# Kernel tuning notes

Measured on AMD Instinct MI355X. Metric: run time of the kernel, lower is better.

The kernel has to match this reference:

```python
import jax, jax.numpy as jnp
import numpy as np

B, DV, DT, H, G, E = 4096, 1024, 1024, 1024, 4096, 8
D = DV + DT  # fused dim = 2048


def setup_inputs() -> dict:
    key = jax.random.key(0)
    ks = jax.random.split(key, 8)
    s = 0.02
    return {
        "vision_cls": jax.random.normal(ks[0], (B, DV), jnp.float32),
        "text_cls": jax.random.normal(ks[1], (B, DT), jnp.float32),
        "W1_imm": jax.random.normal(ks[2], (E, D, H), jnp.float32) * s,
        "b1_imm": jnp.zeros((E, H), jnp.float32),
        "W2_imm": jax.random.normal(ks[3], (E, H, 1), jnp.float32) * s,
        "b2_imm": jnp.zeros((E, 1), jnp.float32),
        "W1_gene": jax.random.normal(ks[4], (E, D, H), jnp.float32) * s,
        "b1_gene": jnp.zeros((E, H), jnp.float32),
        "W2_gene": jax.random.normal(ks[5], (E, H, G), jnp.float32) * s,
        "b2_gene": jnp.zeros((E, G), jnp.float32),
        "organ_idx": jax.random.randint(ks[6], (B,), 0, E, jnp.int32),
    }


def reference(vision_cls, text_cls, W1_imm, b1_imm, W2_imm, b2_imm,
              W1_gene, b1_gene, W2_gene, b2_gene, organ_idx):
    # fused features [B, D]
    fused = jnp.concatenate([vision_cls, text_cls], axis=-1)
    # Dense MoE reference: run every organ head on the full batch, then
    # select each sample's routed output (same math as the per-group
    # gather -> MLP -> scatter in the original; dropout is eval-mode identity).
    h_i = jax.nn.relu(jnp.einsum('bd,edh->ebh', fused, W1_imm) + b1_imm[:, None, :])
    imm_all = jnp.einsum('ebh,eh->eb', h_i, W2_imm[:, :, 0]) + b2_imm[:, :1]  # [E,B]
    h_g = jax.nn.relu(jnp.einsum('bd,edh->ebh', fused, W1_gene) + b1_gene[:, None, :])
    gene_all = jnp.einsum('ebh,ehg->ebg', h_g, W2_gene) + b2_gene[:, None, :]  # [E,B,G]
    bidx = jnp.arange(fused.shape[0])
    immune = imm_all[organ_idx, bidx]      # [B]
    gene = gene_all[organ_idx, bidx]       # [B,G] (uniform gene_dim -> no padding needed)
    return immune, gene, vision_cls, text_cls
```

## Files before the change

### kernel.cpp

```cpp
#include <hip/hip_runtime.h>


#define B_N 4096
#define DV  1024
#define DT  1024
#define DD  2048
#define HH  1024
#define GG  4096
#define EE  8
#define BM  128
#define MAXRB 40
#define PERM_N (MAXRB * BM)
#define LDT 40

typedef __bf16 bf16x8 __attribute__((ext_vector_type(8)));
typedef float f32x4 __attribute__((ext_vector_type(4)));
typedef unsigned short u16x4v __attribute__((ext_vector_type(4)));
typedef unsigned short u16x8v __attribute__((ext_vector_type(8)));

#define H_CNT 0
#define H_FIL 8
#define H_OFF 16
#define H_NRB 24
#define H_BLK 32

static __device__ __forceinline__ unsigned short f2bf(float f) {
  unsigned u = __builtin_bit_cast(unsigned, f);
  u += 0x7fffu + ((u >> 16) & 1u);
  return (unsigned short)(u >> 16);
}
static __device__ __forceinline__ float bf2f(unsigned short s) {
  return __builtin_bit_cast(float, (unsigned)s << 16);
}

static __device__ __forceinline__ void gload16(const void* g, void* l) {
  __builtin_amdgcn_global_load_lds(
      (const __attribute__((address_space(1))) unsigned int*)g,
      (__attribute__((address_space(3))) unsigned int*)l, 16, 0, 0);
}

__global__ void s_init(int* hdr, int* perm) {
  int i = blockIdx.x * 256 + threadIdx.x;
  if (i < 128) hdr[i] = 0;
  if (i < PERM_N) perm[i] = -1;
}
__global__ void s_count(const int* organ, int* hdr) {
  int b = blockIdx.x * 256 + threadIdx.x;
  if (b < B_N) atomicAdd(&hdr[H_CNT + organ[b]], 1);
}
__global__ void s_scan(int* hdr) {
  if (blockIdx.x == 0 && threadIdx.x == 0) {
    int acc = 0;
    for (int e = 0; e < EE; ++e) {
      hdr[H_OFF + e] = acc;
      int nb = (hdr[H_CNT + e] + BM - 1) >> 7;
      int rb0 = acc >> 7;
      for (int i = 0; i < nb; ++i) hdr[H_BLK + rb0 + i] = e;
      acc += nb << 7;
    }
    hdr[H_NRB] = acc >> 7;
  }
}
__global__ void s_scatter(const int* organ, int* hdr, int* perm) {
  int b = blockIdx.x * 256 + threadIdx.x;
  if (b < B_N) {
    int e = organ[b];
    int slot = hdr[H_OFF + e] + atomicAdd(&hdr[H_FIL + e], 1);
    perm[slot] = b;
  }
}

__global__ __launch_bounds__(256) void w_cvt(const float* __restrict__ in,
                                             unsigned short* __restrict__ out,
                                             int K, int N) {
  __shared__ unsigned short ls[64][72];
  const int tid = threadIdx.x;
  const int K0 = blockIdx.y << 6, N0 = blockIdx.x << 6;
  const size_t ein = (size_t)blockIdx.z * K * N;
  const int kr = tid >> 4, n0 = (tid & 15) << 2;
#pragma unroll
  for (int p = 0; p < 4; ++p) {
    int k = (p << 4) + kr;
    float4 f = *(const float4*)&in[ein + (size_t)(K0 + k) * N + N0 + n0];
    ls[n0 + 0][k] = f2bf(f.x);
    ls[n0 + 1][k] = f2bf(f.y);
    ls[n0 + 2][k] = f2bf(f.z);
    ls[n0 + 3][k] = f2bf(f.w);
  }
  __syncthreads();
  const int n = tid >> 2, kc = (tid & 3) << 4;
  u16x8v a = *(const u16x8v*)&ls[n][kc];
  u16x8v b = *(const u16x8v*)&ls[n][kc + 8];
  size_t o = (size_t)blockIdx.z * N * K + (size_t)(N0 + n) * K + K0 + kc;
  *(u16x8v*)&out[o] = a;
  *(u16x8v*)&out[o + 8] = b;
}

__global__ void a_build(const float* __restrict__ vis, const float* __restrict__ txt,
                        const int* __restrict__ hdr, const int* __restrict__ perm,
                        unsigned short* __restrict__ Abuf) {
  const int r = blockIdx.x;
  if (r >= hdr[H_NRB] * BM) return;
  const int smp = perm[r];
  const int c = threadIdx.x << 3;
  u16x8v v;
  if (smp >= 0) {
    const float* src = (c < DV) ? vis + (size_t)smp * DV + c
                                : txt + (size_t)smp * DT + (c - DV);
    float4 a = *(const float4*)src, b = *(const float4*)(src + 4);
    v[0] = f2bf(a.x); v[1] = f2bf(a.y); v[2] = f2bf(a.z); v[3] = f2bf(a.w);
    v[4] = f2bf(b.x); v[5] = f2bf(b.y); v[6] = f2bf(b.z); v[7] = f2bf(b.w);
  } else {
#pragma unroll
    for (int i = 0; i < 8; ++i) v[i] = 0;
  }
  *(u16x8v*)&Abuf[(size_t)r * DD + c] = v;
}

__global__ __launch_bounds__(256) void gemm_l1_v1(
    const unsigned short* __restrict__ Abuf,
    const unsigned short* __restrict__ W1i_t, const unsigned short* __restrict__ W1g_t,
    const float* __restrict__ b1i, const float* __restrict__ b1g,
    const int* __restrict__ hdr,
    unsigned short* __restrict__ H1, unsigned short* __restrict__ H2) {
  const int rb = blockIdx.x;
  if (rb >= hdr[H_NRB]) return;
  const int head = blockIdx.y >> 3;
  const int cb = (blockIdx.y & 7) << 7;
  const int e = hdr[H_BLK + rb];
  const unsigned short* Wt = (head ? W1g_t : W1i_t) + (size_t)e * HH * DD;
  const float* bias = (head ? b1g : b1i) + e * HH;
  unsigned short* Hout = head ? H2 : H1;

  __shared__ __align__(16) unsigned short smem[16384];
  const int tid = threadIdx.x;
  const int lane = tid & 63, wave = tid >> 6;
  const int wr = (wave >> 1) << 6, wc = (wave & 1) << 6;
  const int lr = lane & 15, lk = (lane >> 4) << 3;
  const unsigned short* Arow0 = Abuf + (size_t)rb * BM * DD;

  f32x4 acc[4][4];
#pragma unroll
  for (int m = 0; m < 4; ++m)
#pragma unroll
    for (int n = 0; n < 4; ++n) acc[m][n] = (f32x4){0.f, 0.f, 0.f, 0.f};

  for (int k0 = 0; k0 < DD; k0 += 32) {
#pragma unroll
    for (int j = 0; j < 2; ++j) {
      int s = j * 256 + tid;
      int row = s >> 2, kq = (s & 3) << 3;
      gload16(Arow0 + (size_t)row * DD + k0 + kq,
              smem + ((j * 256 + (tid & 192)) << 3));
    }
#pragma unroll
    for (int j = 0; j < 2; ++j) {
      int s = j * 256 + tid;
      int row = s >> 2, kq = (s & 3) << 3;
      gload16(Wt + (size_t)(cb + row) * DD + k0 + kq,
              smem + 4096 + ((j * 256 + (tid & 192)) << 3));
    }
    __syncthreads();
    bf16x8 af[4], bfr[4];
#pragma unroll
    for (int m = 0; m < 4; ++m)
      af[m] = *(const bf16x8*)&smem[(wr + m * 16 + lr) * 32 + lk];
#pragma unroll
    for (int n = 0; n < 4; ++n)
      bfr[n] = *(const bf16x8*)&smem[4096 + (wc + n * 16 + lr) * 32 + lk];
#pragma unroll
    for (int m = 0; m < 4; ++m)
#pragma unroll
      for (int n = 0; n < 4; ++n)
        acc[m][n] = __builtin_amdgcn_mfma_f32_16x16x32_bf16(af[m], bfr[n], acc[m][n], 0, 0, 0);
    __syncthreads();
  }

  const int r0l = wr + ((lane >> 4) << 2);
#pragma unroll
  for (int n = 0; n < 4; ++n) {
    const int col = wc + n * 16 + lr;
    const float bv = bias[cb + col];
#pragma unroll
    for (int m = 0; m < 4; ++m)
#pragma unroll
      for (int v = 0; v < 4; ++v) {
        int row = r0l + m * 16 + v;
        float x = acc[m][n][v] + bv;
        x = x > 0.f ? x : 0.f;
        smem[((row << 7) + col) ^ ((row & 7) << 3)] = f2bf(x);
      }
  }
  __syncthreads();
#pragma unroll
  for (int c = 0; c < 8; ++c) {
    int q = c * 256 + tid;
    int row = q >> 4, ch = q & 15;
    int off = ((row << 7) + (ch << 3)) ^ ((row & 7) << 3);
    u16x8v val = *(const u16x8v*)&smem[off];
    *(u16x8v*)&Hout[(size_t)(rb * BM + row) * HH + cb + (ch << 3)] = val;
  }
}

__global__ __launch_bounds__(256) void gemm_l2_v1(
    const unsigned short* __restrict__ H2, const unsigned short* __restrict__ W2gt,
    const float* __restrict__ b2g, const int* __restrict__ hdr,
    const int* __restrict__ perm, float* __restrict__ outg) {
  const int rb = blockIdx.x;
  if (rb >= hdr[H_NRB]) return;
  const int cb = blockIdx.y << 7;
  const int e = hdr[H_BLK + rb];
  const unsigned short* Wt = W2gt + (size_t)e * GG * HH;

  __shared__ __align__(16) unsigned short smem[16384];
  const int tid = threadIdx.x;
  const int lane = tid & 63, wave = tid >> 6;
  const int wr = (wave >> 1) << 6, wc = (wave & 1) << 6;
  const int lr = lane & 15, lk = (lane >> 4) << 3;
  const unsigned short* Arow0 = H2 + (size_t)rb * BM * HH;

  f32x4 acc[4][4];
#pragma unroll
  for (int m = 0; m < 4; ++m)
#pragma unroll
    for (int n = 0; n < 4; ++n) acc[m][n] = (f32x4){0.f, 0.f, 0.f, 0.f};

  for (int k0 = 0; k0 < HH; k0 += 32) {
#pragma unroll
    for (int j = 0; j < 2; ++j) {
      int s = j * 256 + tid;
      int row = s >> 2, kq = (s & 3) << 3;
      gload16(Arow0 + (size_t)row * HH + k0 + kq,
              smem + ((j * 256 + (tid & 192)) << 3));
    }
#pragma unroll
    for (int j = 0; j < 2; ++j) {
      int s = j * 256 + tid;
      int row = s >> 2, kq = (s & 3) << 3;
      gload16(Wt + (size_t)(cb + row) * HH + k0 + kq,
              smem + 4096 + ((j * 256 + (tid & 192)) << 3));
    }
    __syncthreads();
    bf16x8 af[4], bfr[4];
#pragma unroll
    for (int m = 0; m < 4; ++m)
      af[m] = *(const bf16x8*)&smem[(wr + m * 16 + lr) * 32 + lk];
#pragma unroll
    for (int n = 0; n < 4; ++n)
      bfr[n] = *(const bf16x8*)&smem[4096 + (wc + n * 16 + lr) * 32 + lk];
#pragma unroll
    for (int m = 0; m < 4; ++m)
#pragma unroll
      for (int n = 0; n < 4; ++n)
        acc[m][n] = __builtin_amdgcn_mfma_f32_16x16x32_bf16(af[m], bfr[n], acc[m][n], 0, 0, 0);
    __syncthreads();
  }

  const int r0l = wr + ((lane >> 4) << 2);
#pragma unroll
  for (int n = 0; n < 4; ++n) {
    const int col = wc + n * 16 + lr;
    const float bv = b2g[e * GG + cb + col];
#pragma unroll
    for (int m = 0; m < 4; ++m)
#pragma unroll
      for (int v = 0; v < 4; ++v) {
        int row = r0l + m * 16 + v;
        smem[((row << 7) + col) ^ ((row & 7) << 3)] = f2bf(acc[m][n][v] + bv);
      }
  }
  __syncthreads();
#pragma unroll
  for (int c = 0; c < 8; ++c) {
    int q = c * 256 + tid;
    int row = q >> 4, ch = q & 15;
    int sm = perm[rb * BM + row];
    if (sm < 0) continue;
    int off = ((row << 7) + (ch << 3)) ^ ((row & 7) << 3);
    u16x8v val = *(const u16x8v*)&smem[off];
    float4 f0, f1;
    f0.x = bf2f(val[0]); f0.y = bf2f(val[1]); f0.z = bf2f(val[2]); f0.w = bf2f(val[3]);
    f1.x = bf2f(val[4]); f1.y = bf2f(val[5]); f1.z = bf2f(val[6]); f1.w = bf2f(val[7]);
    float* dst = outg + (size_t)sm * GG + cb + (ch << 3);
    *(float4*)dst = f0;
    *(float4*)(dst + 4) = f1;
  }
}

__global__ __launch_bounds__(256) void immune_k(
    const int* __restrict__ hdr, const int* __restrict__ perm,
    const unsigned short* __restrict__ H1, const float* __restrict__ W2,
    const float* __restrict__ b2, float* __restrict__ out) {
  const int nrb = hdr[H_NRB];
  const int r = blockIdx.x * 4 + (threadIdx.x >> 6);
  if (r >= nrb * BM) return;
  const int b = perm[r];
  if (b < 0) return;
  const int e = hdr[H_BLK + (r >> 7)];
  const int lane = threadIdx.x & 63;
  const unsigned short* h = H1 + (size_t)r * HH + lane * 16;
  const float* w = W2 + (size_t)e * HH + lane * 16;
  float s = 0.f;
#pragma unroll
  for (int i = 0; i < 16; ++i) s += bf2f(h[i]) * w[i];
#pragma unroll
  for (int off = 32; off >= 1; off >>= 1) s += __shfl_xor(s, off, 64);
  if (lane == 0) out[b] = s + b2[e];
}

__global__ void copy_vt(const float4* __restrict__ v, const float4* __restrict__ t,
                        float4* __restrict__ ov, float4* __restrict__ ot) {
  const int n4 = B_N * DV / 4;
  for (int i = blockIdx.x * blockDim.x + threadIdx.x; i < n4;
       i += gridDim.x * blockDim.x) {
    ov[i] = v[i];
    ot[i] = t[i];
  }
}

__global__ __launch_bounds__(256) void gemm_l1_v0(
    const float* __restrict__ vis, const float* __restrict__ txt,
    const float* __restrict__ W1, const float* __restrict__ b1,
    const int* __restrict__ hdr, const int* __restrict__ perm,
    unsigned short* __restrict__ Hout) {
  const int nrb = hdr[H_NRB];
  const int rb = blockIdx.x;
  if (rb >= nrb) return;
  const int cb = blockIdx.y << 7;
  const int e = hdr[H_BLK + rb];
  const int tid = threadIdx.x;
  __shared__ unsigned short As[BM * LDT];
  __shared__ unsigned short Bs[BM * LDT];
  const int ar = tid & 127, akg = (tid >> 7) << 4;
  const int smp = perm[rb * BM + ar];
  const int bc = (tid & 31) << 2, bk = (tid >> 5) << 2;
  const float* Wb = W1 + (size_t)e * DD * HH;
  const int wave = tid >> 6, lane = tid & 63;
  const int wr = (wave >> 1) << 6, wc = (wave & 1) << 6;
  const int lr = lane & 15, lk = (lane >> 4) << 3;
  f32x4 acc[4][4];
#pragma unroll
  for (int m = 0; m < 4; ++m)
#pragma unroll
    for (int n = 0; n < 4; ++n) acc[m][n] = (f32x4){0.f, 0.f, 0.f, 0.f};
  for (int k0 = 0; k0 < DD; k0 += 32) {
    {
      const int kk = k0 + akg;
      u16x8v v0, v1;
      if (smp >= 0) {
        const float* src = (kk < DV) ? (vis + (size_t)smp * DV + kk)
                                     : (txt + (size_t)smp * DT + (kk - DV));
#pragma unroll
        for (int i = 0; i < 2; ++i) {
          float4 f = reinterpret_cast<const float4*>(src)[i];
          v0[4 * i + 0] = f2bf(f.x); v0[4 * i + 1] = f2bf(f.y);
          v0[4 * i + 2] = f2bf(f.z); v0[4 * i + 3] = f2bf(f.w);
        }
#pragma unroll
        for (int i = 0; i < 2; ++i) {
          float4 f = reinterpret_cast<const float4*>(src)[2 + i];
          v1[4 * i + 0] = f2bf(f.x); v1[4 * i + 1] = f2bf(f.y);
          v1[4 * i + 2] = f2bf(f.z); v1[4 * i + 3] = f2bf(f.w);
        }
      } else {
#pragma unroll
        for (int i = 0; i < 8; ++i) { v0[i] = 0; v1[i] = 0; }
      }
      *reinterpret_cast<u16x8v*>(&As[ar * LDT + akg]) = v0;
      *reinterpret_cast<u16x8v*>(&As[ar * LDT + akg + 8]) = v1;
    }
    {
      unsigned short bv[4][4];
#pragma unroll
      for (int i = 0; i < 4; ++i) {
        float4 f = *reinterpret_cast<const float4*>(Wb + (size_t)(k0 + bk + i) * HH + cb + bc);
        bv[0][i] = f2bf(f.x); bv[1][i] = f2bf(f.y);
        bv[2][i] = f2bf(f.z); bv[3][i] = f2bf(f.w);
      }
#pragma unroll
      for (int j = 0; j < 4; ++j) {
        u16x4v w; w[0] = bv[j][0]; w[1] = bv[j][1]; w[2] = bv[j][2]; w[3] = bv[j][3];
        *reinterpret_cast<u16x4v*>(&Bs[(bc + j) * LDT + bk]) = w;
      }
    }
    __syncthreads();
    bf16x8 af[4], bfr[4];
#pragma unroll
    for (int m = 0; m < 4; ++m)
      af[m] = *reinterpret_cast<const bf16x8*>(&As[(wr + m * 16 + lr) * LDT + lk]);
#pragma unroll
    for (int n = 0; n < 4; ++n)
      bfr[n] = *reinterpret_cast<const bf16x8*>(&Bs[(wc + n * 16 + lr) * LDT + lk]);
#pragma unroll
    for (int m = 0; m < 4; ++m)
#pragma unroll
      for (int n = 0; n < 4; ++n)
        acc[m][n] = __builtin_amdgcn_mfma_f32_16x16x32_bf16(af[m], bfr[n], acc[m][n], 0, 0, 0);
    __syncthreads();
  }
  const int r0 = rb * BM + wr + ((lane >> 4) << 2);
#pragma unroll
  for (int n = 0; n < 4; ++n) {
    const int col = cb + wc + n * 16 + lr;
    const float bias = b1[e * HH + col];
#pragma unroll
    for (int m = 0; m < 4; ++m)
#pragma unroll
      for (int v = 0; v < 4; ++v) {
        float x = acc[m][n][v] + bias;
        x = x > 0.f ? x : 0.f;
        Hout[(size_t)(r0 + m * 16 + v) * HH + col] = f2bf(x);
      }
  }
}

__global__ __launch_bounds__(256) void gemm_l2_v0(
    const unsigned short* __restrict__ H2, const float* __restrict__ W2,
    const float* __restrict__ b2, const int* __restrict__ hdr,
    const int* __restrict__ perm, float* __restrict__ outg) {
  const int nrb = hdr[H_NRB];
  const int rb = blockIdx.x;
  if (rb >= nrb) return;
  const int cb = blockIdx.y << 7;
  const int e = hdr[H_BLK + rb];
  const int tid = threadIdx.x;
  __shared__ unsigned short As[BM * LDT];
  __shared__ unsigned short Bs[BM * LDT];
  const int ar = tid & 127, akg = (tid >> 7) << 4;
  const unsigned short* Arow = H2 + (size_t)(rb * BM + ar) * HH;
  const int bc = (tid & 31) << 2, bk = (tid >> 5) << 2;
  const float* Wb = W2 + (size_t)e * HH * GG;
  const int wave = tid >> 6, lane = tid & 63;
  const int wr = (wave >> 1) << 6, wc = (wave & 1) << 6;
  const int lr = lane & 15, lk = (lane >> 4) << 3;
  f32x4 acc[4][4];
#pragma unroll
  for (int m = 0; m < 4; ++m)
#pragma unroll
    for (int n = 0; n < 4; ++n) acc[m][n] = (f32x4){0.f, 0.f, 0.f, 0.f};
  for (int k0 = 0; k0 < HH; k0 += 32) {
    {
      u16x8v v0 = *reinterpret_cast<const u16x8v*>(Arow + k0 + akg);
      u16x8v v1 = *reinterpret_cast<const u16x8v*>(Arow + k0 + akg + 8);
      *reinterpret_cast<u16x8v*>(&As[ar * LDT + akg]) = v0;
      *reinterpret_cast<u16x8v*>(&As[ar * LDT + akg + 8]) = v1;
    }
    {
      unsigned short bv[4][4];
#pragma unroll
      for (int i = 0; i < 4; ++i) {
        float4 f = *reinterpret_cast<const float4*>(Wb + (size_t)(k0 + bk + i) * GG + cb + bc);
        bv[0][i] = f2bf(f.x); bv[1][i] = f2bf(f.y);
        bv[2][i] = f2bf(f.z); bv[3][i] = f2bf(f.w);
      }
#pragma unroll
      for (int j = 0; j < 4; ++j) {
        u16x4v w; w[0] = bv[j][0]; w[1] = bv[j][1]; w[2] = bv[j][2]; w[3] = bv[j][3];
        *reinterpret_cast<u16x4v*>(&Bs[(bc + j) * LDT + bk]) = w;
      }
    }
    __syncthreads();
    bf16x8 af[4], bfr[4];
#pragma unroll
    for (int m = 0; m < 4; ++m)
      af[m] = *reinterpret_cast<const bf16x8*>(&As[(wr + m * 16 + lr) * LDT + lk]);
#pragma unroll
    for (int n = 0; n < 4; ++n)
      bfr[n] = *reinterpret_cast<const bf16x8*>(&Bs[(wc + n * 16 + lr) * LDT + lk]);
#pragma unroll
    for (int m = 0; m < 4; ++m)
#pragma unroll
      for (int n = 0; n < 4; ++n)
        acc[m][n] = __builtin_amdgcn_mfma_f32_16x16x32_bf16(af[m], bfr[n], acc[m][n], 0, 0, 0);
    __syncthreads();
  }
  const int r0 = rb * BM + wr + ((lane >> 4) << 2);
#pragma unroll
  for (int m = 0; m < 4; ++m) {
    int sm[4];
#pragma unroll
    for (int v = 0; v < 4; ++v) sm[v] = perm[r0 + m * 16 + v];
#pragma unroll
    for (int n = 0; n < 4; ++n) {
      const int col = cb + wc + n * 16 + lr;
      const float bias = b2[e * GG + col];
#pragma unroll
      for (int v = 0; v < 4; ++v)
        if (sm[v] >= 0) outg[(size_t)sm[v] * GG + col] = acc[m][n][v] + bias;
    }
  }
}

extern "C" void kernel_launch(void* const* d_in, const int* in_sizes, int n_in,
                              void* d_out, int out_size, void* d_ws, size_t ws_size,
                              hipStream_t stream) {
  (void)in_sizes; (void)n_in; (void)out_size;
  const float* vis = (const float*)d_in[0];
  const float* txt = (const float*)d_in[1];
  const float* W1i = (const float*)d_in[2];
  const float* b1i = (const float*)d_in[3];
  const float* W2i = (const float*)d_in[4];
  const float* b2i = (const float*)d_in[5];
  const float* W1g = (const float*)d_in[6];
  const float* b1g = (const float*)d_in[7];
  const float* W2g = (const float*)d_in[8];
  const float* b2g = (const float*)d_in[9];
  const int* organ = (const int*)d_in[10];

  float* out_imm = (float*)d_out;
  float* out_gene = out_imm + B_N;
  float* out_vis = out_gene + (size_t)B_N * GG;
  float* out_txt = out_vis + (size_t)B_N * DV;

  int* hdr = (int*)d_ws;
  int* perm = hdr + 128;

  const size_t OFF_ABUF = 32768;
  const size_t OFF_H1 = OFF_ABUF + (size_t)PERM_N * DD * 2;
  const size_t OFF_H2 = OFF_H1 + (size_t)PERM_N * HH * 2;
  const size_t OFF_W1I = OFF_H2 + (size_t)PERM_N * HH * 2;
  const size_t OFF_W1G = OFF_W1I + (size_t)EE * HH * DD * 2;
  const size_t OFF_W2G = OFF_W1G + (size_t)EE * HH * DD * 2;
  const size_t NEED = OFF_W2G + (size_t)EE * GG * HH * 2;

  s_init<<<PERM_N / 256, 256, 0, stream>>>(hdr, perm);
  s_count<<<B_N / 256, 256, 0, stream>>>(organ, hdr);
  s_scan<<<1, 64, 0, stream>>>(hdr);
  s_scatter<<<B_N / 256, 256, 0, stream>>>(organ, hdr, perm);

  if (ws_size >= NEED) {
    unsigned short* Abuf = (unsigned short*)((char*)d_ws + OFF_ABUF);
    unsigned short* H1 = (unsigned short*)((char*)d_ws + OFF_H1);
    unsigned short* H2 = (unsigned short*)((char*)d_ws + OFF_H2);
    unsigned short* W1i_t = (unsigned short*)((char*)d_ws + OFF_W1I);
    unsigned short* W1g_t = (unsigned short*)((char*)d_ws + OFF_W1G);
    unsigned short* W2g_t = (unsigned short*)((char*)d_ws + OFF_W2G);

    w_cvt<<<dim3(HH / 64, DD / 64, EE), 256, 0, stream>>>(W1i, W1i_t, DD, HH);
    w_cvt<<<dim3(HH / 64, DD / 64, EE), 256, 0, stream>>>(W1g, W1g_t, DD, HH);
    w_cvt<<<dim3(GG / 64, HH / 64, EE), 256, 0, stream>>>(W2g, W2g_t, HH, GG);
    a_build<<<PERM_N, 256, 0, stream>>>(vis, txt, hdr, perm, Abuf);

    gemm_l1_v1<<<dim3(MAXRB, 16), 256, 0, stream>>>(Abuf, W1i_t, W1g_t, b1i, b1g,
                                                    hdr, H1, H2);
    immune_k<<<PERM_N / 4, 256, 0, stream>>>(hdr, perm, H1, W2i, b2i, out_imm);
    gemm_l2_v1<<<dim3(MAXRB, GG / 128), 256, 0, stream>>>(H2, W2g_t, b2g, hdr,
                                                          perm, out_gene);
  } else {
    unsigned short* H1 = (unsigned short*)((char*)d_ws + 32768);
    unsigned short* H2 = H1 + (size_t)PERM_N * HH;
    gemm_l1_v0<<<dim3(MAXRB, HH / 128), 256, 0, stream>>>(vis, txt, W1i, b1i, hdr, perm, H1);
    gemm_l1_v0<<<dim3(MAXRB, HH / 128), 256, 0, stream>>>(vis, txt, W1g, b1g, hdr, perm, H2);
    immune_k<<<PERM_N / 4, 256, 0, stream>>>(hdr, perm, H1, W2i, b2i, out_imm);
    gemm_l2_v0<<<dim3(MAXRB, GG / 128), 256, 0, stream>>>(H2, W2g, b2g, hdr, perm, out_gene);
  }
  copy_vt<<<2048, 256, 0, stream>>>((const float4*)vis, (const float4*)txt,
                                    (float4*)out_vis, (float4*)out_txt);
}
```

Baseline: 311.6 us.

## Merge launches into fused multi-role kernels and double-buffer GEMM main loop

```diff
diff --git a/kernel.cpp b/kernel.cpp
--- a/kernel.cpp
+++ b/kernel.cpp
@@ -32,112 +32,171 @@
 static __device__ __forceinline__ float bf2f(unsigned short s) {
   return __builtin_bit_cast(float, (unsigned)s << 16);
 }
-
 static __device__ __forceinline__ void gload16(const void* g, void* l) {
   __builtin_amdgcn_global_load_lds(
       (const __attribute__((address_space(1))) unsigned int*)g,
       (__attribute__((address_space(3))) unsigned int*)l, 16, 0, 0);
 }
 
-__global__ void s_init(int* hdr, int* perm) {
-  int i = blockIdx.x * 256 + threadIdx.x;
-  if (i < 128) hdr[i] = 0;
-  if (i < PERM_N) perm[i] = -1;
-}
-__global__ void s_count(const int* organ, int* hdr) {
-  int b = blockIdx.x * 256 + threadIdx.x;
-  if (b < B_N) atomicAdd(&hdr[H_CNT + organ[b]], 1);
-}
-__global__ void s_scan(int* hdr) {
-  if (blockIdx.x == 0 && threadIdx.x == 0) {
+__global__ __launch_bounds__(1024) void routing(const int* __restrict__ organ,
+                                                int* __restrict__ hdr,
+                                                int* __restrict__ perm) {
+  __shared__ int cnt[EE], fil[EE], off[EE];
+  const int tid = threadIdx.x;
+  if (tid < EE) { cnt[tid] = 0; fil[tid] = 0; }
+  __syncthreads();
+#pragma unroll
+  for (int i = 0; i < 4; ++i) atomicAdd(&cnt[organ[tid + (i << 10)]], 1);
+#pragma unroll
+  for (int i = 0; i < 5; ++i) perm[tid + (i << 10)] = -1;
+  __syncthreads();
+  if (tid == 0) {
     int acc = 0;
     for (int e = 0; e < EE; ++e) {
+      off[e] = acc;
       hdr[H_OFF + e] = acc;
-      int nb = (hdr[H_CNT + e] + BM - 1) >> 7;
+      hdr[H_CNT + e] = cnt[e];
+      int nb = (cnt[e] + BM - 1) >> 7;
       int rb0 = acc >> 7;
       for (int i = 0; i < nb; ++i) hdr[H_BLK + rb0 + i] = e;
       acc += nb << 7;
     }
     hdr[H_NRB] = acc >> 7;
   }
-}
-__global__ void s_scatter(const int* organ, int* hdr, int* perm) {
-  int b = blockIdx.x * 256 + threadIdx.x;
-  if (b < B_N) {
+  __syncthreads();
+#pragma unroll
+  for (int i = 0; i < 4; ++i) {
+    int b = tid + (i << 10);
     int e = organ[b];
-    int slot = hdr[H_OFF + e] + atomicAdd(&hdr[H_FIL + e], 1);
+    int slot = off[e] + atomicAdd(&fil[e], 1);
     perm[slot] = b;
   }
 }
 
-__global__ __launch_bounds__(256) void w_cvt(const float* __restrict__ in,
-                                             unsigned short* __restrict__ out,
-                                             int K, int N) {
-  __shared__ unsigned short ls[64][72];
-  const int tid = threadIdx.x;
-  const int K0 = blockIdx.y << 6, N0 = blockIdx.x << 6;
-  const size_t ein = (size_t)blockIdx.z * K * N;
+static __device__ __forceinline__ void wcvt_body(
+    const float* __restrict__ in, unsigned short* __restrict__ out,
+    int K, int N, int bx, unsigned short* ls) {
+  const int nn = N >> 6, nk = K >> 6;
+  const int e = bx / (nk * nn);
+  int rem = bx - e * nk * nn;
+  const int K0 = (rem / nn) << 6, N0 = (rem % nn) << 6;
+  const size_t ein = (size_t)e * K * N;
+  const int tid = threadIdx.x;
   const int kr = tid >> 4, n0 = (tid & 15) << 2;
 #pragma unroll
   for (int p = 0; p < 4; ++p) {
     int k = (p << 4) + kr;
     float4 f = *(const float4*)&in[ein + (size_t)(K0 + k) * N + N0 + n0];
-    ls[n0 + 0][k] = f2bf(f.x);
-    ls[n0 + 1][k] = f2bf(f.y);
-    ls[n0 + 2][k] = f2bf(f.z);
-    ls[n0 + 3][k] = f2bf(f.w);
+    ls[(n0 + 0) * 72 + k] = f2bf(f.x);
+    ls[(n0 + 1) * 72 + k] = f2bf(f.y);
+    ls[(n0 + 2) * 72 + k] = f2bf(f.z);
+    ls[(n0 + 3) * 72 + k] = f2bf(f.w);
   }
   __syncthreads();
   const int n = tid >> 2, kc = (tid & 3) << 4;
-  u16x8v a = *(const u16x8v*)&ls[n][kc];
-  u16x8v b = *(const u16x8v*)&ls[n][kc + 8];
-  size_t o = (size_t)blockIdx.z * N * K + (size_t)(N0 + n) * K + K0 + kc;
+  u16x8v a = *(const u16x8v*)&ls[n * 72 + kc];
+  u16x8v b = *(const u16x8v*)&ls[n * 72 + kc + 8];
+  size_t o = (size_t)e * N * K + (size_t)(N0 + n) * K + K0 + kc;
   *(u16x8v*)&out[o] = a;
   *(u16x8v*)&out[o + 8] = b;
 }
 
-__global__ void a_build(const float* __restrict__ vis, const float* __restrict__ txt,
-                        const int* __restrict__ hdr, const int* __restrict__ perm,
-                        unsigned short* __restrict__ Abuf) {
-  const int r = blockIdx.x;
-  if (r >= hdr[H_NRB] * BM) return;
-  const int smp = perm[r];
-  const int c = threadIdx.x << 3;
-  u16x8v v;
-  if (smp >= 0) {
-    const float* src = (c < DV) ? vis + (size_t)smp * DV + c
-                                : txt + (size_t)smp * DT + (c - DV);
-    float4 a = *(const float4*)src, b = *(const float4*)(src + 4);
-    v[0] = f2bf(a.x); v[1] = f2bf(a.y); v[2] = f2bf(a.z); v[3] = f2bf(a.w);
-    v[4] = f2bf(b.x); v[5] = f2bf(b.y); v[6] = f2bf(b.z); v[7] = f2bf(b.w);
-  } else {
-#pragma unroll
-    for (int i = 0; i < 8; ++i) v[i] = 0;
-  }
-  *(u16x8v*)&Abuf[(size_t)r * DD + c] = v;
-}
-
-__global__ __launch_bounds__(256) void gemm_l1_v1(
-    const unsigned short* __restrict__ Abuf,
+static __device__ __forceinline__ void abuild_body(
+    int bx, const float* __restrict__ vis, const float* __restrict__ txt,
+    const int* __restrict__ hdr, const int* __restrict__ perm,
+    unsigned short* __restrict__ Abuf) {
+  const int nr = hdr[H_NRB] << 7;
+  const int tid = threadIdx.x;
+  const int c = tid << 3;
+  const float* srcbase = (c < DV) ? vis : txt;
+  const int cc = (c < DV) ? c : c - DV;
+#pragma unroll
+  for (int p = 0; p < 4; ++p) {
+    int r = (bx << 2) + p;
+    if (r >= nr) return;
+    int smp = perm[r];
+    u16x8v v;
+    if (smp >= 0) {
+      const float* src = srcbase + (size_t)smp * 1024 + cc;
+      float4 a = *(const float4*)src, b = *(const float4*)(src + 4);
+      v[0] = f2bf(a.x); v[1] = f2bf(a.y); v[2] = f2bf(a.z); v[3] = f2bf(a.w);
+      v[4] = f2bf(b.x); v[5] = f2bf(b.y); v[6] = f2bf(b.z); v[7] = f2bf(b.w);
+    } else {
+#pragma unroll
+      for (int i = 0; i < 8; ++i) v[i] = 0;
+    }
+    *(u16x8v*)&Abuf[(size_t)r * DD + c] = v;
+  }
+}
+
+template <int KDIM>
+static __device__ __forceinline__ void gemm_main(
+    const unsigned short* __restrict__ Aseg,
+    const unsigned short* __restrict__ Bseg,
+    unsigned short* smem, f32x4 (&acc)[4][4]) {
+  const int tid = threadIdx.x;
+  const int lane = tid & 63, wave = tid >> 6;
+  const int wr = (wave >> 1) << 6, wc = (wave & 1) << 6;
+  const int lr = lane & 15, lk = (lane >> 4) << 3;
+  const int j0row = tid >> 2;
+  const int kq = (tid & 3) << 3;
+  const int wbase = (tid & 192) << 3;
+  constexpr int NT = KDIM / 32;
+
+  auto stage = [&](int buf, int k0) {
+#pragma unroll
+    for (int j = 0; j < 2; ++j) {
+      const int row = (j << 6) + j0row;
+      gload16(Aseg + (size_t)row * KDIM + k0 + kq,
+              smem + (buf << 12) + (j << 11) + wbase);
+      gload16(Bseg + (size_t)row * KDIM + k0 + kq,
+              smem + 8192 + (buf << 12) + (j << 11) + wbase);
+    }
+  };
+
+  stage(0, 0);
+  asm volatile("s_waitcnt vmcnt(0)" ::: "memory");
+  __syncthreads();
+#pragma unroll 2
+  for (int kt = 0; kt < NT; ++kt) {
+    const int cur = kt & 1;
+    if (kt + 1 < NT) stage(cur ^ 1, (kt + 1) << 5);
+    bf16x8 af[4], bfr[4];
+#pragma unroll
+    for (int m = 0; m < 4; ++m)
+      af[m] = *(const bf16x8*)&smem[(cur << 12) + (wr + m * 16 + lr) * 32 + lk];
+#pragma unroll
+    for (int n = 0; n < 4; ++n)
+      bfr[n] = *(const bf16x8*)&smem[8192 + (cur << 12) + (wc + n * 16 + lr) * 32 + lk];
+#pragma unroll
+    for (int m = 0; m < 4; ++m)
+#pragma unroll
+      for (int n = 0; n < 4; ++n)
+        acc[m][n] = __builtin_amdgcn_mfma_f32_16x16x32_bf16(af[m], bfr[n], acc[m][n], 0, 0, 0);
+    asm volatile("s_waitcnt vmcnt(0)" ::: "memory");
+    __syncthreads();
+  }
+}
+
+static __device__ void gemm_l1_body(
+    int bx, const unsigned short* __restrict__ Abuf,
     const unsigned short* __restrict__ W1i_t, const unsigned short* __restrict__ W1g_t,
     const float* __restrict__ b1i, const float* __restrict__ b1g,
-    const int* __restrict__ hdr,
-    unsigned short* __restrict__ H1, unsigned short* __restrict__ H2) {
-  const int rb = blockIdx.x;
+    const int* __restrict__ hdr, unsigned short* __restrict__ H1,
+    unsigned short* __restrict__ H2, unsigned short* smem) {
+  const int rb = bx % MAXRB;
+  const int cy = bx / MAXRB;
   if (rb >= hdr[H_NRB]) return;
-  const int head = blockIdx.y >> 3;
-  const int cb = (blockIdx.y & 7) << 7;
+  const int head = cy >> 3;
+  const int cb = (cy & 7) << 7;
   const int e = hdr[H_BLK + rb];
   const unsigned short* Wt = (head ? W1g_t : W1i_t) + (size_t)e * HH * DD;
   const float* bias = (head ? b1g : b1i) + e * HH;
   unsigned short* Hout = head ? H2 : H1;
-
-  __shared__ __align__(16) unsigned short smem[16384];
   const int tid = threadIdx.x;
   const int lane = tid & 63, wave = tid >> 6;
   const int wr = (wave >> 1) << 6, wc = (wave & 1) << 6;
-  const int lr = lane & 15, lk = (lane >> 4) << 3;
-  const unsigned short* Arow0 = Abuf + (size_t)rb * BM * DD;
+  const int lr = lane & 15;
 
   f32x4 acc[4][4];
 #pragma unroll
@@ -145,36 +204,7 @@
 #pragma unroll
     for (int n = 0; n < 4; ++n) acc[m][n] = (f32x4){0.f, 0.f, 0.f, 0.f};
 
-  for (int k0 = 0; k0 < DD; k0 += 32) {
-#pragma unroll
-    for (int j = 0; j < 2; ++j) {
-      int s = j * 256 + tid;
-      int row = s >> 2, kq = (s & 3) << 3;
-      gload16(Arow0 + (size_t)row * DD + k0 + kq,
-              smem + ((j * 256 + (tid & 192)) << 3));
-    }
-#pragma unroll
-    for (int j = 0; j < 2; ++j) {
-      int s = j * 256 + tid;
-      int row = s >> 2, kq = (s & 3) << 3;
-      gload16(Wt + (size_t)(cb + row) * DD + k0 + kq,
-              smem + 4096 + ((j * 256 + (tid & 192)) << 3));
-    }
-    __syncthreads();
-    bf16x8 af[4], bfr[4];
-#pragma unroll
-    for (int m = 0; m < 4; ++m)
-      af[m] = *(const bf16x8*)&smem[(wr + m * 16 + lr) * 32 + lk];
-#pragma unroll
-    for (int n = 0; n < 4; ++n)
-      bfr[n] = *(const bf16x8*)&smem[4096 + (wc + n * 16 + lr) * 32 + lk];
-#pragma unroll
-    for (int m = 0; m < 4; ++m)
-#pragma unroll
-      for (int n = 0; n < 4; ++n)
-        acc[m][n] = __builtin_amdgcn_mfma_f32_16x16x32_bf16(af[m], bfr[n], acc[m][n], 0, 0, 0);
-    __syncthreads();
-  }
+  gemm_main<DD>(Abuf + (size_t)rb * BM * DD, Wt + (size_t)cb * DD, smem, acc);
 
   const int r0l = wr + ((lane >> 4) << 2);
 #pragma unroll
@@ -202,22 +232,19 @@
   }
 }
 
-__global__ __launch_bounds__(256) void gemm_l2_v1(
-    const unsigned short* __restrict__ H2, const unsigned short* __restrict__ W2gt,
-    const float* __restrict__ b2g, const int* __restrict__ hdr,
-    const int* __restrict__ perm, float* __restrict__ outg) {
-  const int rb = blockIdx.x;
+static __device__ void gemm_l2_body(
+    int bx, const unsigned short* __restrict__ H2buf,
+    const unsigned short* __restrict__ W2gt, const float* __restrict__ b2g,
+    const int* __restrict__ hdr, const int* __restrict__ perm,
+    float* __restrict__ outg, unsigned short* smem) {
+  const int rb = bx % MAXRB;
+  const int cb = (bx / MAXRB) << 7;
   if (rb >= hdr[H_NRB]) return;
-  const int cb = blockIdx.y << 7;
   const int e = hdr[H_BLK + rb];
-  const unsigned short* Wt = W2gt + (size_t)e * GG * HH;
-
-  __shared__ __align__(16) unsigned short smem[16384];
   const int tid = threadIdx.x;
   const int lane = tid & 63, wave = tid >> 6;
   const int wr = (wave >> 1) << 6, wc = (wave & 1) << 6;
-  const int lr = lane & 15, lk = (lane >> 4) << 3;
-  const unsigned short* Arow0 = H2 + (size_t)rb * BM * HH;
+  const int lr = lane & 15;
 
   f32x4 acc[4][4];
 #pragma unroll
@@ -225,36 +252,8 @@
 #pragma unroll
     for (int n = 0; n < 4; ++n) acc[m][n] = (f32x4){0.f, 0.f, 0.f, 0.f};
 
-  for (int k0 = 0; k0 < HH; k0 += 32) {
-#pragma unroll
-    for (int j = 0; j < 2; ++j) {
-      int s = j * 256 + tid;
-      int row = s >> 2, kq = (s & 3) << 3;
-      gload16(Arow0 + (size_t)row * HH + k0 + kq,
-              smem + ((j * 256 + (tid & 192)) << 3));
-    }
-#pragma unroll
-    for (int j = 0; j < 2; ++j) {
-      int s = j * 256 + tid;
-      int row = s >> 2, kq = (s & 3) << 3;
-      gload16(Wt + (size_t)(cb + row) * HH + k0 + kq,
-              smem + 4096 + ((j * 256 + (tid & 192)) << 3));
-    }
-    __syncthreads();
-    bf16x8 af[4], bfr[4];
-#pragma unroll
-    for (int m = 0; m < 4; ++m)
-      af[m] = *(const bf16x8*)&smem[(wr + m * 16 + lr) * 32 + lk];
-#pragma unroll
-    for (int n = 0; n < 4; ++n)
-      bfr[n] = *(const bf16x8*)&smem[4096 + (wc + n * 16 + lr) * 32 + lk];
-#pragma unroll
-    for (int m = 0; m < 4; ++m)
-#pragma unroll
-      for (int n = 0; n < 4; ++n)
-        acc[m][n] = __builtin_amdgcn_mfma_f32_16x16x32_bf16(af[m], bfr[n], acc[m][n], 0, 0, 0);
-    __syncthreads();
-  }
+  gemm_main<HH>(H2buf + (size_t)rb * BM * HH,
+                W2gt + (size_t)e * GG * HH + (size_t)cb * HH, smem, acc);
 
   const int r0l = wr + ((lane >> 4) << 2);
 #pragma unroll
@@ -287,12 +286,12 @@
   }
 }
 
-__global__ __launch_bounds__(256) void immune_k(
-    const int* __restrict__ hdr, const int* __restrict__ perm,
+static __device__ __forceinline__ void immune_body(
+    int bx, const int* __restrict__ hdr, const int* __restrict__ perm,
     const unsigned short* __restrict__ H1, const float* __restrict__ W2,
     const float* __restrict__ b2, float* __restrict__ out) {
   const int nrb = hdr[H_NRB];
-  const int r = blockIdx.x * 4 + (threadIdx.x >> 6);
+  const int r = bx * 4 + (threadIdx.x >> 6);
   if (r >= nrb * BM) return;
   const int b = perm[r];
   if (b < 0) return;
@@ -308,14 +307,75 @@
   if (lane == 0) out[b] = s + b2[e];
 }
 
-__global__ void copy_vt(const float4* __restrict__ v, const float4* __restrict__ t,
-                        float4* __restrict__ ov, float4* __restrict__ ot) {
+static __device__ __forceinline__ void copy_body(
+    int bx, const float4* __restrict__ v, const float4* __restrict__ t,
+    float4* __restrict__ ov, float4* __restrict__ ot) {
   const int n4 = B_N * DV / 4;
-  for (int i = blockIdx.x * blockDim.x + threadIdx.x; i < n4;
-       i += gridDim.x * blockDim.x) {
+  for (int i = bx * 256 + (int)threadIdx.x; i < n4; i += 1024 * 256) {
     ov[i] = v[i];
     ot[i] = t[i];
   }
+}
+
+#define G_CVT1 (EE * (DD >> 6) * (HH >> 6))
+#define G_AB   (PERM_N / 4)
+#define G_L1   (MAXRB * 16)
+#define G_CVT2 (EE * (HH >> 6) * (GG >> 6))
+#define G_COPY 1024
+#define G_L2   (MAXRB * 32)
+#define G_IMM  (PERM_N / 4)
+
+__global__ __launch_bounds__(256) void k_prep(
+    const float* __restrict__ W1i, const float* __restrict__ W1g,
+    unsigned short* __restrict__ W1i_t, unsigned short* __restrict__ W1g_t,
+    const float* __restrict__ vis, const float* __restrict__ txt,
+    const int* __restrict__ hdr, const int* __restrict__ perm,
+    unsigned short* __restrict__ Abuf) {
+  __shared__ __align__(16) unsigned short sm[64 * 72];
+  int bx = blockIdx.x;
+  if (bx < G_CVT1) { wcvt_body(W1i, W1i_t, DD, HH, bx, sm); return; }
+  bx -= G_CVT1;
+  if (bx < G_CVT1) { wcvt_body(W1g, W1g_t, DD, HH, bx, sm); return; }
+  bx -= G_CVT1;
+  abuild_body(bx, vis, txt, hdr, perm, Abuf);
+}
+
+__global__ __launch_bounds__(256) void k_main1(
+    const unsigned short* __restrict__ Abuf,
+    const unsigned short* __restrict__ W1i_t, const unsigned short* __restrict__ W1g_t,
+    const float* __restrict__ b1i, const float* __restrict__ b1g,
+    const int* __restrict__ hdr, unsigned short* __restrict__ H1,
+    unsigned short* __restrict__ H2, const float* __restrict__ W2g,
+    unsigned short* __restrict__ W2g_t, const float4* __restrict__ vis4,
+    const float4* __restrict__ txt4, float4* __restrict__ ov,
+    float4* __restrict__ ot) {
+  __shared__ __align__(16) unsigned short smem[16384];
+  int bx = blockIdx.x;
+  if (bx < G_L1) {
+    gemm_l1_body(bx, Abuf, W1i_t, W1g_t, b1i, b1g, hdr, H1, H2, smem);
+    return;
+  }
+  bx -= G_L1;
+  if (bx < G_CVT2) { wcvt_body(W2g, W2g_t, HH, GG, bx, smem); return; }
+  bx -= G_CVT2;
+  copy_body(bx, vis4, txt4, ov, ot);
+}
+
+__global__ __launch_bounds__(256) void k_main2(
+    const unsigned short* __restrict__ H2buf,
+    const unsigned short* __restrict__ W2gt, const float* __restrict__ b2g,
+    const int* __restrict__ hdr, const int* __restrict__ perm,
+    float* __restrict__ outg, const unsigned short* __restrict__ H1,
+    const float* __restrict__ W2i, const float* __restrict__ b2i,
+    float* __restrict__ outi) {
+  __shared__ __align__(16) unsigned short smem[16384];
+  int bx = blockIdx.x;
+  if (bx < G_L2) {
+    gemm_l2_body(bx, H2buf, W2gt, b2g, hdr, perm, outg, smem);
+    return;
+  }
+  bx -= G_L2;
+  immune_body(bx, hdr, perm, H1, W2i, b2i, outi);
 }
 
 __global__ __launch_bounds__(256) void gemm_l1_v0(
@@ -489,6 +549,18 @@
         if (sm[v] >= 0) outg[(size_t)sm[v] * GG + col] = acc[m][n][v] + bias;
     }
   }
+}
+
+__global__ __launch_bounds__(256) void immune_k(
+    const int* __restrict__ hdr, const int* __restrict__ perm,
+    const unsigned short* __restrict__ H1, const float* __restrict__ W2,
+    const float* __restrict__ b2, float* __restrict__ out) {
+  immune_body(blockIdx.x, hdr, perm, H1, W2, b2, out);
+}
+
+__global__ void copy_vt(const float4* __restrict__ v, const float4* __restrict__ t,
+                        float4* __restrict__ ov, float4* __restrict__ ot) {
+  copy_body(blockIdx.x, v, t, ov, ot);
 }
 
 extern "C" void kernel_launch(void* const* d_in, const int* in_sizes, int n_in,
@@ -523,10 +595,7 @@
   const size_t OFF_W2G = OFF_W1G + (size_t)EE * HH * DD * 2;
   const size_t NEED = OFF_W2G + (size_t)EE * GG * HH * 2;
 
-  s_init<<<PERM_N / 256, 256, 0, stream>>>(hdr, perm);
-  s_count<<<B_N / 256, 256, 0, stream>>>(organ, hdr);
-  s_scan<<<1, 64, 0, stream>>>(hdr);
-  s_scatter<<<B_N / 256, 256, 0, stream>>>(organ, hdr, perm);
+  routing<<<1, 1024, 0, stream>>>(organ, hdr, perm);
 
   if (ws_size >= NEED) {
     unsigned short* Abuf = (unsigned short*)((char*)d_ws + OFF_ABUF);
@@ -536,16 +605,14 @@
     unsigned short* W1g_t = (unsigned short*)((char*)d_ws + OFF_W1G);
     unsigned short* W2g_t = (unsigned short*)((char*)d_ws + OFF_W2G);
 
-    w_cvt<<<dim3(HH / 64, DD / 64, EE), 256, 0, stream>>>(W1i, W1i_t, DD, HH);
-    w_cvt<<<dim3(HH / 64, DD / 64, EE), 256, 0, stream>>>(W1g, W1g_t, DD, HH);
-    w_cvt<<<dim3(GG / 64, HH / 64, EE), 256, 0, stream>>>(W2g, W2g_t, HH, GG);
-    a_build<<<PERM_N, 256, 0, stream>>>(vis, txt, hdr, perm, Abuf);
-
-    gemm_l1_v1<<<dim3(MAXRB, 16), 256, 0, stream>>>(Abuf, W1i_t, W1g_t, b1i, b1g,
-                                                    hdr, H1, H2);
-    immune_k<<<PERM_N / 4, 256, 0, stream>>>(hdr, perm, H1, W2i, b2i, out_imm);
-    gemm_l2_v1<<<dim3(MAXRB, GG / 128), 256, 0, stream>>>(H2, W2g_t, b2g, hdr,
-                                                          perm, out_gene);
+    k_prep<<<G_CVT1 * 2 + G_AB, 256, 0, stream>>>(W1i, W1g, W1i_t, W1g_t, vis,
+                                                  txt, hdr, perm, Abuf);
+    k_main1<<<G_L1 + G_CVT2 + G_COPY, 256, 0, stream>>>(
+        Abuf, W1i_t, W1g_t, b1i, b1g, hdr, H1, H2, W2g, W2g_t,
+        (const float4*)vis, (const float4*)txt, (float4*)out_vis,
+        (float4*)out_txt);
+    k_main2<<<G_L2 + G_IMM, 256, 0, stream>>>(H2, W2g_t, b2g, hdr, perm,
+                                              out_gene, H1, W2i, b2i, out_imm);
   } else {
     unsigned short* H1 = (unsigned short*)((char*)d_ws + 32768);
     unsigned short* H2 = H1 + (size_t)PERM_N * HH;
@@ -553,7 +620,7 @@
     gemm_l1_v0<<<dim3(MAXRB, HH / 128), 256, 0, stream>>>(vis, txt, W1g, b1g, hdr, perm, H2);
     immune_k<<<PERM_N / 4, 256, 0, stream>>>(hdr, perm, H1, W2i, b2i, out_imm);
     gemm_l2_v0<<<dim3(MAXRB, GG / 128), 256, 0, stream>>>(H2, W2g, b2g, hdr, perm, out_gene);
-  }
-  copy_vt<<<2048, 256, 0, stream>>>((const float4*)vis, (const float4*)txt,
-                                    (float4*)out_vis, (float4*)out_txt);
-}
+    copy_vt<<<G_COPY, 256, 0, stream>>>((const float4*)vis, (const float4*)txt,
+                                        (float4*)out_vis, (float4*)out_txt);
+  }
+}
```

New measurement: 253.7 us. 1.23x faster.
